# Performance work log

Measured on AMD Instinct MI355X. Metric: run time of the kernel, lower is better.

Reference implementation:

```python
import math
import jax, jax.numpy as jnp
import numpy as np

EPS = 1e-5
TEMP = 1.0
ROPE_BASE = 10000.0


def _ln(x, g, b):
    m = x.mean(-1, keepdims=True)
    v = ((x - m) ** 2).mean(-1, keepdims=True)
    return (x - m) / jnp.sqrt(v + EPS) * g + b


def _trigrams(n_heads):
    # 8 trigrams = all sign patterns of {-1,+1}^3, L2-normalized rows
    bits = ((np.arange(8)[:, None] >> np.arange(3)[None, :]) & 1).astype(np.float32)
    t = bits * 2.0 - 1.0
    t = t / np.linalg.norm(t, axis=1, keepdims=True)
    return jnp.asarray(t[:n_heads])  # [H, 3]


def _rope_tables(T, D):
    inv = 1.0 / (ROPE_BASE ** (np.arange(0, D, 2, dtype=np.float32) / D))
    ang = np.arange(T, dtype=np.float32)[:, None] * inv[None, :]  # [T, D/2]
    cos = np.concatenate([np.cos(ang), np.cos(ang)], axis=1)  # [T, D]
    sin = np.concatenate([np.sin(ang), np.sin(ang)], axis=1)
    return jnp.asarray(cos), jnp.asarray(sin)


def _apply_rope(x, cos, sin):
    # x: [B, H, T, D], rotate-half convention
    d = x.shape[-1] // 2
    rot = jnp.concatenate([-x[..., d:], x[..., :d]], axis=-1)
    return x * cos + rot * sin


def setup_inputs() -> dict:
    key = jax.random.key(0)
    ks = jax.random.split(key, 8)
    B, T, C, H = 2, 2048, 1024, 8
    FFN, QD = 4096, 6
    w = 0.02
    return {
        "x": jax.random.normal(ks[0], (B, T, C), jnp.float32),
        "ln_attn_g": jnp.ones((C,), jnp.float32),
        "ln_attn_b": jnp.zeros((C,), jnp.float32),
        "qkv_w": jax.random.normal(ks[1], (3 * C, C), jnp.float32) * w,
        "out_w": jax.random.normal(ks[2], (C, C), jnp.float32) * w,
        "head_scales": jax.random.normal(ks[3], (H,), jnp.float32) * 0.1,
        "ln_hex_g": jnp.ones((C,), jnp.float32),
        "ln_hex_b": jnp.zeros((C,), jnp.float32),
        "to_qd_w": jax.random.normal(ks[4], (QD, C), jnp.float32) * w,
        "from_qd_w": jax.random.normal(ks[5], (C, QD), jnp.float32) * w,
        "hex_scale": jnp.ones((1,), jnp.float32),
        "ln_ffn_g": jnp.ones((C,), jnp.float32),
        "ln_ffn_b": jnp.zeros((C,), jnp.float32),
        "ffn_w1": jax.random.normal(ks[6], (FFN, C), jnp.float32) * w,
        "ffn_b1": jnp.zeros((FFN,), jnp.float32),
        "ffn_w2": jax.random.normal(ks[7], (C, FFN), jnp.float32) * w,
        "ffn_b2": jnp.zeros((C,), jnp.float32),
    }


def _layer(x, ln_attn_g, ln_attn_b, qkv_w, out_w, head_scales,
           ln_hex_g, ln_hex_b, to_qd_w, from_qd_w, hex_scale,
           ln_ffn_g, ln_ffn_b, ffn_w1, ffn_b1, ffn_w2, ffn_b2):
    B, T, C = x.shape
    H = head_scales.shape[0]
    D = C // H

    # ---- attention with trigram geo-bias ----
    h = _ln(x, ln_attn_g, ln_attn_b)
    qkv = (h @ qkv_w.T).reshape(B, T, 3, H, D).transpose(2, 0, 3, 1, 4)
    q, k, v = qkv[0], qkv[1], qkv[2]  # [B, H, T, D]
    cos, sin = _rope_tables(T, D)
    q = _apply_rope(q, cos, sin)
    k = _apply_rope(k, cos, sin)

    mask = jnp.tril(jnp.ones((T, T), bool))
    scale = jnp.float32(1.0 / math.sqrt(D))
    scores = jnp.einsum('bhtd,bhsd->bhts', q, k) * scale
    scores = jnp.where(mask, scores, -jnp.inf)
    attn = jax.nn.softmax(scores, axis=-1)
    out = attn @ v  # [B, H, T, D]

    # rank-1 geometric correction (flash path)
    dirs = _trigrams(H)  # [H, 3]
    qp = jnp.einsum('bhtd,hd->bht', q[..., :3], dirs)
    kp = jnp.einsum('bhtd,hd->bht', k[..., :3], dirs)
    geo = qp[..., :, None] * kp[..., None, :]  # [B, H, T, T]
    geo_attn = jax.nn.softmax(jnp.where(mask, geo, -jnp.inf), axis=-1)
    geo_out = geo_attn @ v
    out = out + head_scales[None, :, None, None] * jax.lax.stop_gradient(geo_out - out)

    out = out.transpose(0, 2, 1, 3).reshape(B, T, C) @ out_w.T
    x = x + out

    # ---- hexagram VQ (factored6: per-dim binary quantize w/ straight-through) ----
    h = _ln(x, ln_hex_g, ln_hex_b)
    zq = h @ to_qd_w.T  # [B, T, 6]
    soft = jnp.tanh(zq / TEMP)
    hard = jnp.where(zq >= 0, 1.0, -1.0).astype(zq.dtype)
    zq_out = soft + jax.lax.stop_gradient(hard - soft)
    x = x + hex_scale[0] * (zq_out @ from_qd_w.T)

    # ---- FFN (GELU) ----
    h = _ln(x, ln_ffn_g, ln_ffn_b)
    x = x + (jax.nn.gelu(h @ ffn_w1.T + ffn_b1, approximate=False) @ ffn_w2.T + ffn_b2)
    return x


def reference(x, ln_attn_g, ln_attn_b, qkv_w, out_w, head_scales,
              ln_hex_g, ln_hex_b, to_qd_w, from_qd_w, hex_scale,
              ln_ffn_g, ln_ffn_b, ffn_w1, ffn_b1, ffn_w2, ffn_b2):
    return _layer(x, ln_attn_g, ln_attn_b, qkv_w, out_w, head_scales,
                  ln_hex_g, ln_hex_b, to_qd_w, from_qd_w, hex_scale,
                  ln_ffn_g, ln_ffn_b, ffn_w1, ffn_b1, ffn_w2, ffn_b2)
```

## Files before the change

### kernel.cpp

```cpp
#include <hip/hip_runtime.h>
#include <hip/hip_bf16.h>

typedef __attribute__((ext_vector_type(4))) float f32x4;
typedef __attribute__((ext_vector_type(8))) short short8;
typedef __attribute__((ext_vector_type(4))) short short4v;

namespace {

constexpr int Tt = 2048, Cc = 1024, Hh = 8, Dd = 128, FFNd = 4096;
constexpr int Bb = 2;
constexpr int Mrows = Bb * Tt;
constexpr float kNEG = -1e30f;
constexpr float L2E = 1.4426950408889634f;

static __device__ __forceinline__ float b2f(unsigned short u) {
  return __uint_as_float(((unsigned int)u) << 16);
}
static __device__ __forceinline__ unsigned short f2b(float f) {
  __hip_bfloat16 h = __float2bfloat16(f);
  unsigned short u;
  __builtin_memcpy(&u, &h, 2);
  return u;
}
static __device__ __forceinline__ void split2(float v, unsigned short& h, unsigned short& l) {
  h = f2b(v);
  float r = v - b2f(h);
  l = f2b(r);
}
static __device__ __forceinline__ void split3(float v, unsigned short& h, unsigned short& m,
                                              unsigned short& l) {
  h = f2b(v);
  float r = v - b2f(h);
  m = f2b(r);
  float r2 = r - b2f(m);
  l = f2b(r2);
}
static __device__ __forceinline__ float wave_sum(float v) {
#pragma unroll
  for (int m = 1; m < 64; m <<= 1) v += __shfl_xor(v, m);
  return v;
}
static __device__ __forceinline__ float grp16_sum(float v) {
#pragma unroll
  for (int m = 1; m < 16; m <<= 1) v += __shfl_xor(v, m);
  return v;
}
static __device__ __forceinline__ float grp16_max(float v) {
#pragma unroll
  for (int m = 1; m < 16; m <<= 1) v = fmaxf(v, __shfl_xor(v, m));
  return v;
}

__global__ __launch_bounds__(256) void cast_kernel(const float* __restrict__ in,
                                                   unsigned short* __restrict__ out, int n) {
  int i = (blockIdx.x * 256 + threadIdx.x) * 4;
  if (i + 3 < n) {
    float4 v = *(const float4*)&in[i];
    short4v o;
    o.x = (short)f2b(v.x);
    o.y = (short)f2b(v.y);
    o.z = (short)f2b(v.z);
    o.w = (short)f2b(v.w);
    *(short4v*)&out[i] = o;
  }
}

__global__ __launch_bounds__(256) void ln_kernel(const float* __restrict__ x,
                                                 const float* __restrict__ g,
                                                 const float* __restrict__ bb,
                                                 float* __restrict__ out) {
  int row = blockIdx.x * 4 + (threadIdx.x >> 6);
  int lane = threadIdx.x & 63;
  const float* xr = x + (size_t)row * Cc;
  float v[16];
  float s = 0.f;
#pragma unroll
  for (int c = 0; c < 4; ++c) {
    float4 t = *(const float4*)&xr[c * 256 + lane * 4];
    v[c * 4 + 0] = t.x; v[c * 4 + 1] = t.y; v[c * 4 + 2] = t.z; v[c * 4 + 3] = t.w;
    s += t.x + t.y + t.z + t.w;
  }
  s = wave_sum(s);
  float mean = s * (1.f / Cc);
  float s2 = 0.f;
#pragma unroll
  for (int j = 0; j < 16; ++j) {
    float d = v[j] - mean;
    s2 += d * d;
  }
  s2 = wave_sum(s2);
  float rstd = 1.0f / sqrtf(s2 * (1.f / Cc) + 1e-5f);
#pragma unroll
  for (int c = 0; c < 4; ++c) {
    float4 o;
#pragma unroll
    for (int j = 0; j < 4; ++j) {
      int idx = c * 256 + lane * 4 + j;
      ((float*)&o)[j] = (v[c * 4 + j] - mean) * rstd * g[idx] + bb[idx];
    }
    *(float4*)&out[(size_t)row * Cc + c * 256 + lane * 4] = o;
  }
}

template <int NS, int EPI>
__global__ __launch_bounds__(256) void gemm_sp(const float* __restrict__ A,
                                               const float* __restrict__ W,
                                               float* __restrict__ outF,
                                               unsigned short* __restrict__ outH,
                                               unsigned short* __restrict__ outL,
                                               const float* __restrict__ resid, int Nn, int Kk) {
  __shared__ __align__(16) unsigned short As[NS][128 * 32];
  __shared__ __align__(16) unsigned short Bs[NS][128 * 32];
  int m0 = blockIdx.x * 128, n0 = blockIdx.y * 128;
  int tid = threadIdx.x, lane = tid & 63, wid = tid >> 6;
  int wr = (wid >> 1) * 64, wc = (wid & 1) * 64;
  int g = lane >> 4, r16 = lane & 15;
  f32x4 acc[4][4];
#pragma unroll
  for (int mi = 0; mi < 4; ++mi)
#pragma unroll
    for (int ni = 0; ni < 4; ++ni) acc[mi][ni] = (f32x4){0.f, 0.f, 0.f, 0.f};
  for (int k0 = 0; k0 < Kk; k0 += 32) {
    __syncthreads();
#pragma unroll
    for (int it = 0; it < 4; ++it) {
      int chunk = tid + it * 256;
      int row = chunk >> 3, col4 = chunk & 7;
      int cc = col4 >> 1, half = col4 & 1;
      int off = row * 32 + ((cc ^ (row & 3)) * 8) + half * 4;
      float4 va = *(const float4*)&A[(size_t)(m0 + row) * Kk + k0 + col4 * 4];
      float4 vb = *(const float4*)&W[(size_t)(n0 + row) * Kk + k0 + col4 * 4];
      short4v sa[NS], sb[NS];
#pragma unroll
      for (int j = 0; j < 4; ++j) {
        unsigned short h, m, l;
        if constexpr (NS == 2) {
          split2(((float*)&va)[j], h, l);
          ((short*)&sa[0])[j] = (short)h; ((short*)&sa[1])[j] = (short)l;
          split2(((float*)&vb)[j], h, l);
          ((short*)&sb[0])[j] = (short)h; ((short*)&sb[1])[j] = (short)l;
        } else {
          split3(((float*)&va)[j], h, m, l);
          ((short*)&sa[0])[j] = (short)h; ((short*)&sa[1])[j] = (short)m; ((short*)&sa[2])[j] = (short)l;
          split3(((float*)&vb)[j], h, m, l);
          ((short*)&sb[0])[j] = (short)h; ((short*)&sb[1])[j] = (short)m; ((short*)&sb[2])[j] = (short)l;
        }
      }
#pragma unroll
      for (int s = 0; s < NS; ++s) {
        *(short4v*)&As[s][off] = sa[s];
        *(short4v*)&Bs[s][off] = sb[s];
      }
    }
    __syncthreads();
    short8 af[NS][4], bfv[NS][4];
#pragma unroll
    for (int mi = 0; mi < 4; ++mi) {
      int row = wr + mi * 16 + r16;
      int so = row * 32 + ((g ^ (row & 3)) * 8);
#pragma unroll
      for (int s = 0; s < NS; ++s) af[s][mi] = *(short8*)&As[s][so];
    }
#pragma unroll
    for (int ni = 0; ni < 4; ++ni) {
      int row = wc + ni * 16 + r16;
      int so = row * 32 + ((g ^ (row & 3)) * 8);
#pragma unroll
      for (int s = 0; s < NS; ++s) bfv[s][ni] = *(short8*)&Bs[s][so];
    }
    __builtin_amdgcn_s_setprio(1);
#pragma unroll
    for (int mi = 0; mi < 4; ++mi)
#pragma unroll
      for (int ni = 0; ni < 4; ++ni) {
        f32x4 a = acc[mi][ni];
        if constexpr (NS == 3) {
          a = __builtin_amdgcn_mfma_f32_16x16x32_bf16(af[1][mi], bfv[1][ni], a, 0, 0, 0);
          a = __builtin_amdgcn_mfma_f32_16x16x32_bf16(af[0][mi], bfv[2][ni], a, 0, 0, 0);
          a = __builtin_amdgcn_mfma_f32_16x16x32_bf16(af[2][mi], bfv[0][ni], a, 0, 0, 0);
        }
        a = __builtin_amdgcn_mfma_f32_16x16x32_bf16(af[0][mi], bfv[1][ni], a, 0, 0, 0);
        a = __builtin_amdgcn_mfma_f32_16x16x32_bf16(af[1][mi], bfv[0][ni], a, 0, 0, 0);
        a = __builtin_amdgcn_mfma_f32_16x16x32_bf16(af[0][mi], bfv[0][ni], a, 0, 0, 0);
        acc[mi][ni] = a;
      }
    __builtin_amdgcn_s_setprio(0);
  }
#pragma unroll
  for (int mi = 0; mi < 4; ++mi)
#pragma unroll
    for (int ni = 0; ni < 4; ++ni)
#pragma unroll
      for (int r = 0; r < 4; ++r) {
        int row = m0 + wr + mi * 16 + 4 * g + r;
        int col = n0 + wc + ni * 16 + r16;
        size_t o = (size_t)row * Nn + col;
        float v = acc[mi][ni][r];
        if constexpr (EPI == 0) {
          outF[o] = v;
        } else if constexpr (EPI == 1) {
          outF[o] = v + resid[o];
        } else {
          unsigned short hh, ll;
          split2(v, hh, ll);
          outH[o] = hh;
          outL[o] = ll;
        }
      }
}

template <int EPI>
__global__ __launch_bounds__(256) void gemm_bt(const unsigned short* __restrict__ A,
                                               const unsigned short* __restrict__ W,
                                               float* __restrict__ outF,
                                               unsigned short* __restrict__ outB,
                                               const float* __restrict__ bias,
                                               const float* __restrict__ resid, int Nn, int Kk) {
  __shared__ __align__(16) unsigned short As[128 * 32];
  __shared__ __align__(16) unsigned short Bs[128 * 32];
  int m0 = blockIdx.x * 128, n0 = blockIdx.y * 128;
  int tid = threadIdx.x, lane = tid & 63, wid = tid >> 6;
  int wr = (wid >> 1) * 64, wc = (wid & 1) * 64;
  int g = lane >> 4, r16 = lane & 15;
  f32x4 acc[4][4];
#pragma unroll
  for (int mi = 0; mi < 4; ++mi)
#pragma unroll
    for (int ni = 0; ni < 4; ++ni) acc[mi][ni] = (f32x4){0.f, 0.f, 0.f, 0.f};
  for (int k0 = 0; k0 < Kk; k0 += 32) {
    __syncthreads();
#pragma unroll
    for (int c = 0; c < 2; ++c) {
      int chunk = tid + c * 256;
      int row = chunk >> 2, cc = chunk & 3;
      int sw = cc ^ (row & 3);
      *(short8*)&As[row * 32 + sw * 8] = *(const short8*)&A[(size_t)(m0 + row) * Kk + k0 + cc * 8];
      *(short8*)&Bs[row * 32 + sw * 8] = *(const short8*)&W[(size_t)(n0 + row) * Kk + k0 + cc * 8];
    }
    __syncthreads();
    short8 af[4], bfr[4];
#pragma unroll
    for (int mi = 0; mi < 4; ++mi) {
      int row = wr + mi * 16 + r16;
      af[mi] = *(short8*)&As[row * 32 + ((g ^ (row & 3)) * 8)];
    }
#pragma unroll
    for (int ni = 0; ni < 4; ++ni) {
      int row = wc + ni * 16 + r16;
      bfr[ni] = *(short8*)&Bs[row * 32 + ((g ^ (row & 3)) * 8)];
    }
    __builtin_amdgcn_s_setprio(1);
#pragma unroll
    for (int mi = 0; mi < 4; ++mi)
#pragma unroll
      for (int ni = 0; ni < 4; ++ni)
        acc[mi][ni] = __builtin_amdgcn_mfma_f32_16x16x32_bf16(af[mi], bfr[ni], acc[mi][ni], 0, 0, 0);
    __builtin_amdgcn_s_setprio(0);
  }
#pragma unroll
  for (int mi = 0; mi < 4; ++mi)
#pragma unroll
    for (int ni = 0; ni < 4; ++ni)
#pragma unroll
      for (int r = 0; r < 4; ++r) {
        int row = m0 + wr + mi * 16 + 4 * g + r;
        int col = n0 + wc + ni * 16 + r16;
        size_t o = (size_t)row * Nn + col;
        float v = acc[mi][ni][r];
        if constexpr (EPI == 2) {
          v += bias[col];
          v = 0.5f * v * (1.f + erff(v * 0.70710678118654752f));
          outB[o] = f2b(v);
        } else {
          v += bias[col];
          outF[o] = v + resid[o];
        }
      }
}

__global__ __launch_bounds__(256) void rope_table(float* __restrict__ ct, float* __restrict__ st) {
  int idx = blockIdx.x * 256 + threadIdx.x;
  int t = idx >> 6, i = idx & 63;
  float e = (float)i * (1.f / 64.f);
  float p = powf(10000.0f, e);
  float inv = 1.0f / p;
  float ang = (float)t * inv;
  ct[idx] = cosf(ang);
  st[idx] = sinf(ang);
}

__global__ __launch_bounds__(256) void rope_apply(unsigned short* __restrict__ qkvh,
                                                  unsigned short* __restrict__ qkvl,
                                                  unsigned short* __restrict__ khsw,
                                                  unsigned short* __restrict__ klsw,
                                                  const float* __restrict__ ct,
                                                  const float* __restrict__ st,
                                                  float* __restrict__ qp, float* __restrict__ kp) {
  int w = blockIdx.x * 4 + (threadIdx.x >> 6);
  int lane = threadIdx.x & 63;
  int b = w / (Hh * Tt);
  int rem = w % (Hh * Tt);
  int h = rem / Tt;
  int t = rem % Tt;
  size_t base = ((size_t)(b * Tt + t)) * 3 * Cc + h * Dd;
  float cv = ct[t * 64 + lane], sv = st[t * 64 + lane];
  float q_lo = b2f(qkvh[base + lane]) + b2f(qkvl[base + lane]);
  float q_hi = b2f(qkvh[base + lane + 64]) + b2f(qkvl[base + lane + 64]);
  float qn_lo = q_lo * cv - q_hi * sv;
  float qn_hi = q_hi * cv + q_lo * sv;
  unsigned short hh, ll;
  split2(qn_lo, hh, ll);
  qkvh[base + lane] = hh; qkvl[base + lane] = ll;
  split2(qn_hi, hh, ll);
  qkvh[base + lane + 64] = hh; qkvl[base + lane + 64] = ll;
  size_t kbase = base + Cc;
  float k_lo = b2f(qkvh[kbase + lane]) + b2f(qkvl[kbase + lane]);
  float k_hi = b2f(qkvh[kbase + lane + 64]) + b2f(qkvl[kbase + lane + 64]);
  float kn_lo = k_lo * cv - k_hi * sv;
  float kn_hi = k_hi * cv + k_lo * sv;
  size_t krow = ((size_t)(b * Hh + h) * Tt + t) * 128;
  int tsw = t & 7;
  int d0 = lane, d1 = lane + 64;
  int c0 = (((d0 >> 3) ^ tsw) << 3) | (d0 & 7);
  int c1 = (((d1 >> 3) ^ tsw) << 3) | (d1 & 7);
  split2(kn_lo, hh, ll);
  khsw[krow + c0] = hh; klsw[krow + c0] = ll;
  split2(kn_hi, hh, ll);
  khsw[krow + c1] = hh; klsw[krow + c1] = ll;
  float t0 = (((h >> 0) & 1) ? 1.f : -1.f) * 0.57735026918962576f;
  float t1 = (((h >> 1) & 1) ? 1.f : -1.f) * 0.57735026918962576f;
  float t2 = (((h >> 2) & 1) ? 1.f : -1.f) * 0.57735026918962576f;
  float q0v = __shfl(qn_lo, 0), q1v = __shfl(qn_lo, 1), q2v = __shfl(qn_lo, 2);
  float k0v = __shfl(kn_lo, 0), k1v = __shfl(kn_lo, 1), k2v = __shfl(kn_lo, 2);
  if (lane == 0) {
    qp[(size_t)(b * Hh + h) * Tt + t] = q0v * t0 + q1v * t1 + q2v * t2;
    kp[(size_t)(b * Hh + h) * Tt + t] = k0v * t0 + k1v * t1 + k2v * t2;
  }
}

__global__ __launch_bounds__(256) void vtrans(const unsigned short* __restrict__ qkvh,
                                              const unsigned short* __restrict__ qkvl,
                                              unsigned short* __restrict__ vth,
                                              unsigned short* __restrict__ vtl) {
  __shared__ unsigned short Lh[64 * 68], Ll[64 * 68];
  int bidx = blockIdx.x;
  int dd = bidx & 1;
  int tt = (bidx >> 1) & 31;
  int bh = bidx >> 6;
  int b = bh >> 3, h = bh & 7;
  int tid = threadIdx.x;
#pragma unroll
  for (int it = 0; it < 2; ++it) {
    int chunk = tid + it * 256;
    int tr = chunk >> 3, c8 = chunk & 7;
    size_t src = ((size_t)(b * Tt + tt * 64 + tr)) * 3 * Cc + 2 * Cc + h * Dd + dd * 64 + c8 * 8;
    short8 vh = *(const short8*)&qkvh[src];
    short8 vl = *(const short8*)&qkvl[src];
    *(short4v*)&Lh[tr * 68 + c8 * 8] = *(short4v*)&vh;
    *(short4v*)&Lh[tr * 68 + c8 * 8 + 4] = *((short4v*)&vh + 1);
    *(short4v*)&Ll[tr * 68 + c8 * 8] = *(short4v*)&vl;
    *(short4v*)&Ll[tr * 68 + c8 * 8 + 4] = *((short4v*)&vl + 1);
  }
  __syncthreads();
#pragma unroll
  for (int it = 0; it < 2; ++it) {
    int chunk = tid + it * 256;
    int dr = chunk >> 3, t8 = chunk & 7;
    short8 oh, ol;
#pragma unroll
    for (int e = 0; e < 8; ++e) {
      oh[e] = (short)Lh[(t8 * 8 + e) * 68 + dr];
      ol[e] = (short)Ll[(t8 * 8 + e) * 68 + dr];
    }
    size_t dst = ((size_t)(bh * Dd + dd * 64 + dr)) * Tt + tt * 64 + t8 * 8;
    *(short8*)&vth[dst] = oh;
    *(short8*)&vtl[dst] = ol;
  }
}

__global__ __launch_bounds__(256) void attn_fused(const unsigned short* __restrict__ qkvh,
                                                  const unsigned short* __restrict__ qkvl,
                                                  const unsigned short* __restrict__ khsw,
                                                  const unsigned short* __restrict__ klsw,
                                                  const unsigned short* __restrict__ vth,
                                                  const unsigned short* __restrict__ vtl,
                                                  const float* __restrict__ qp,
                                                  const float* __restrict__ kp,
                                                  const float* __restrict__ head_scales,
                                                  float* __restrict__ out) {
  int i = blockIdx.x;
  int bh = i & 15;
  int j = i >> 4;
  int qblk = (j < 16) ? (31 - j) : (j - 16);
  int b = bh >> 3, h = bh & 7;
  int q0 = qblk * 64;
  int tid = threadIdx.x, lane = tid & 63, wid = tid >> 6;
  int wq0 = q0 + wid * 16;
  int g = lane >> 4, r16 = lane & 15;
  __shared__ __align__(16) unsigned short Ksh[32 * 128], Ksl[32 * 128];
  __shared__ __align__(16) unsigned short Vsh[128 * 40], Vsl[128 * 40];
  __shared__ __align__(16) unsigned short PsAh[4][512], PsAl[4][512];
  __shared__ __align__(16) unsigned short PsGh[4][512], PsGl[4][512];

  short8 qh[4], ql[4];
#pragma unroll
  for (int c = 0; c < 4; ++c) {
    size_t qoff = (size_t)(b * Tt + wq0 + r16) * 3 * Cc + h * Dd + c * 32 + g * 8;
    qh[c] = *(const short8*)&qkvh[qoff];
    ql[c] = *(const short8*)&qkvl[qoff];
  }

  float hs = head_scales[h];
  const float* qpb = qp + (size_t)bh * Tt;
  const float* kpb = kp + (size_t)bh * Tt;
  float qpv[4];
#pragma unroll
  for (int r = 0; r < 4; ++r) qpv[r] = qpb[wq0 + 4 * g + r] * L2E;

  f32x4 accA[8], accG[8];
#pragma unroll
  for (int n = 0; n < 8; ++n) {
    accA[n] = (f32x4){0.f, 0.f, 0.f, 0.f};
    accG[n] = (f32x4){0.f, 0.f, 0.f, 0.f};
  }
  float m1[4], l1[4], m2[4], l2[4];
#pragma unroll
  for (int r = 0; r < 4; ++r) { m1[r] = kNEG; l1[r] = 0.f; m2[r] = kNEG; l2[r] = 0.f; }

  const float scale2 = 0.08838834764831845f * L2E;

  const unsigned short* Khb = khsw + (size_t)bh * Tt * 128;
  const unsigned short* Klb = klsw + (size_t)bh * Tt * 128;
  const unsigned short* Vhb = vth + (size_t)bh * Dd * Tt;
  const unsigned short* Vlb = vtl + (size_t)bh * Dd * Tt;

  for (int s0 = 0; s0 < q0 + 64; s0 += 32) {
    __syncthreads();
#pragma unroll
    for (int it = 0; it < 2; ++it) {
      int chunk = tid + it * 256;
      int row = chunk >> 4, c8 = chunk & 15;
      size_t src = (size_t)(s0 + row) * 128 + c8 * 8;
      *(short8*)&Ksh[row * 128 + c8 * 8] = *(const short8*)&Khb[src];
      *(short8*)&Ksl[row * 128 + c8 * 8] = *(const short8*)&Klb[src];
    }
#pragma unroll
    for (int it = 0; it < 2; ++it) {
      int chunk = tid + it * 256;
      int d = chunk >> 2, k8 = chunk & 3;
      size_t src = (size_t)d * Tt + s0 + k8 * 8;
      *(short8*)&Vsh[d * 40 + k8 * 8] = *(const short8*)&Vhb[src];
      *(short8*)&Vsl[d * 40 + k8 * 8] = *(const short8*)&Vlb[src];
    }
    __syncthreads();
    if (s0 <= wq0 + 15) {
      f32x4 sf[2];
      sf[0] = (f32x4){0.f, 0.f, 0.f, 0.f};
      sf[1] = (f32x4){0.f, 0.f, 0.f, 0.f};
      __builtin_amdgcn_s_setprio(1);
#pragma unroll
      for (int st2 = 0; st2 < 2; ++st2) {
        int row = st2 * 16 + r16;
        int rsw = row & 7;
#pragma unroll
        for (int c = 0; c < 4; ++c) {
          int off = row * 128 + (((c * 4 + g) ^ rsw) * 8);
          short8 kh = *(short8*)&Ksh[off];
          short8 kl = *(short8*)&Ksl[off];
          sf[st2] = __builtin_amdgcn_mfma_f32_16x16x32_bf16(ql[c], kh, sf[st2], 0, 0, 0);
          sf[st2] = __builtin_amdgcn_mfma_f32_16x16x32_bf16(qh[c], kl, sf[st2], 0, 0, 0);
          sf[st2] = __builtin_amdgcn_mfma_f32_16x16x32_bf16(qh[c], kh, sf[st2], 0, 0, 0);
        }
      }
      __builtin_amdgcn_s_setprio(0);
      float kpv2[2];
      kpv2[0] = kpb[s0 + r16];
      kpv2[1] = kpb[s0 + 16 + r16];
      float pA[2][4], pG[2][4], scl1[4], scl2[4];
#pragma unroll
      for (int r = 0; r < 4; ++r) {
        int qi = wq0 + 4 * g + r;
        bool ok0 = (s0 + r16) <= qi;
        bool ok1 = (s0 + 16 + r16) <= qi;
        float sv0 = ok0 ? sf[0][r] * scale2 : kNEG;
        float sv1 = ok1 ? sf[1][r] * scale2 : kNEG;
        float tm = grp16_max(fmaxf(sv0, sv1));
        float mn = fmaxf(m1[r], tm);
        float sc = exp2f(m1[r] - mn);
        float p0 = ok0 ? exp2f(sv0 - mn) : 0.f;
        float p1 = ok1 ? exp2f(sv1 - mn) : 0.f;
        l1[r] = l1[r] * sc + grp16_sum(p0 + p1);
        m1[r] = mn; scl1[r] = sc; pA[0][r] = p0; pA[1][r] = p1;
        float gv0 = qpv[r] * kpv2[0];
        float gv1 = qpv[r] * kpv2[1];
        float g0 = ok0 ? gv0 : kNEG;
        float g1 = ok1 ? gv1 : kNEG;
        float tg = grp16_max(fmaxf(g0, g1));
        float mg = fmaxf(m2[r], tg);
        float sg = exp2f(m2[r] - mg);
        float pg0 = ok0 ? exp2f(g0 - mg) : 0.f;
        float pg1 = ok1 ? exp2f(g1 - mg) : 0.f;
        l2[r] = l2[r] * sg + grp16_sum(pg0 + pg1);
        m2[r] = mg; scl2[r] = sg; pG[0][r] = pg0; pG[1][r] = pg1;
      }
#pragma unroll
      for (int n = 0; n < 8; ++n)
#pragma unroll
        for (int r = 0; r < 4; ++r) {
          accA[n][r] *= scl1[r];
          accG[n][r] *= scl2[r];
        }
#pragma unroll
      for (int st2 = 0; st2 < 2; ++st2)
#pragma unroll
        for (int r = 0; r < 4; ++r) {
          int rowp = 4 * g + r;
          int cbase = st2 * 2 + (r16 >> 3);
          int cs = cbase ^ (rowp & 3);
          int off = rowp * 32 + cs * 8 + (r16 & 7);
          unsigned short hh, ll;
          split2(pA[st2][r], hh, ll);
          PsAh[wid][off] = hh; PsAl[wid][off] = ll;
          split2(pG[st2][r], hh, ll);
          PsGh[wid][off] = hh; PsGl[wid][off] = ll;
        }
      int po = r16 * 32 + ((g ^ (r16 & 3)) * 8);
      short8 aph = *(short8*)&PsAh[wid][po];
      short8 apl = *(short8*)&PsAl[wid][po];
      short8 agh = *(short8*)&PsGh[wid][po];
      short8 agl = *(short8*)&PsGl[wid][po];
      __builtin_amdgcn_s_setprio(1);
#pragma unroll
      for (int n = 0; n < 8; ++n) {
        int vo = (n * 16 + r16) * 40 + g * 8;
        short8 bvh = *(short8*)&Vsh[vo];
        short8 bvl = *(short8*)&Vsl[vo];
        accA[n] = __builtin_amdgcn_mfma_f32_16x16x32_bf16(apl, bvh, accA[n], 0, 0, 0);
        accA[n] = __builtin_amdgcn_mfma_f32_16x16x32_bf16(aph, bvl, accA[n], 0, 0, 0);
        accA[n] = __builtin_amdgcn_mfma_f32_16x16x32_bf16(aph, bvh, accA[n], 0, 0, 0);
        accG[n] = __builtin_amdgcn_mfma_f32_16x16x32_bf16(agl, bvh, accG[n], 0, 0, 0);
        accG[n] = __builtin_amdgcn_mfma_f32_16x16x32_bf16(agh, bvl, accG[n], 0, 0, 0);
        accG[n] = __builtin_amdgcn_mfma_f32_16x16x32_bf16(agh, bvh, accG[n], 0, 0, 0);
      }
      __builtin_amdgcn_s_setprio(0);
    }
  }
#pragma unroll
  for (int n = 0; n < 8; ++n)
#pragma unroll
    for (int r = 0; r < 4; ++r) {
      int qi = wq0 + 4 * g + r;
      float av = accA[n][r] / l1[r];
      float gv = accG[n][r] / l2[r];
      out[(size_t)(b * Tt + qi) * Cc + h * Dd + n * 16 + r16] = av + hs * (gv - av);
    }
}

__global__ __launch_bounds__(256) void hex_kernel(float* __restrict__ x1,
                                                  const float* __restrict__ hg,
                                                  const float* __restrict__ hb,
                                                  const float* __restrict__ to_qd,
                                                  const float* __restrict__ from_qd,
                                                  const float* __restrict__ hex_scale,
                                                  const float* __restrict__ fg,
                                                  const float* __restrict__ fb,
                                                  unsigned short* __restrict__ h_ffn) {
  int row = blockIdx.x * 4 + (threadIdx.x >> 6);
  int lane = threadIdx.x & 63;
  float* xr = x1 + (size_t)row * Cc;
  float v[16];
  float s = 0.f;
#pragma unroll
  for (int c = 0; c < 4; ++c) {
    float4 t = *(const float4*)&xr[c * 256 + lane * 4];
    v[c * 4 + 0] = t.x; v[c * 4 + 1] = t.y; v[c * 4 + 2] = t.z; v[c * 4 + 3] = t.w;
    s += t.x + t.y + t.z + t.w;
  }
  s = wave_sum(s);
  float mean = s * (1.f / Cc);
  float s2 = 0.f;
#pragma unroll
  for (int j = 0; j < 16; ++j) { float d = v[j] - mean; s2 += d * d; }
  s2 = wave_sum(s2);
  float rstd = 1.0f / sqrtf(s2 * (1.f / Cc) + 1e-5f);
  float zq[6] = {0.f, 0.f, 0.f, 0.f, 0.f, 0.f};
#pragma unroll
  for (int c = 0; c < 4; ++c)
#pragma unroll
    for (int j2 = 0; j2 < 4; ++j2) {
      int idx = c * 256 + lane * 4 + j2;
      float hv = (v[c * 4 + j2] - mean) * rstd * hg[idx] + hb[idx];
#pragma unroll
      for (int j = 0; j < 6; ++j) zq[j] += hv * to_qd[j * Cc + idx];
    }
#pragma unroll
  for (int j = 0; j < 6; ++j) zq[j] = wave_sum(zq[j]);
  float hsc = hex_scale[0];
  float hard[6];
#pragma unroll
  for (int j = 0; j < 6; ++j) hard[j] = (zq[j] >= 0.f) ? hsc : -hsc;
  float x2v[16];
  float t1 = 0.f;
#pragma unroll
  for (int c = 0; c < 4; ++c)
#pragma unroll
    for (int j2 = 0; j2 < 4; ++j2) {
      int idx = c * 256 + lane * 4 + j2;
      float a = 0.f;
#pragma unroll
      for (int j = 0; j < 6; ++j) a += hard[j] * from_qd[idx * 6 + j];
      float xv = v[c * 4 + j2] + a;
      x2v[c * 4 + j2] = xv;
      t1 += xv;
    }
  t1 = wave_sum(t1);
  float mean2 = t1 * (1.f / Cc);
  float t2 = 0.f;
#pragma unroll
  for (int j = 0; j < 16; ++j) { float d = x2v[j] - mean2; t2 += d * d; }
  t2 = wave_sum(t2);
  float rstd2 = 1.0f / sqrtf(t2 * (1.f / Cc) + 1e-5f);
#pragma unroll
  for (int c = 0; c < 4; ++c) {
    float4 t;
    t.x = x2v[c * 4 + 0]; t.y = x2v[c * 4 + 1]; t.z = x2v[c * 4 + 2]; t.w = x2v[c * 4 + 3];
    *(float4*)&xr[c * 256 + lane * 4] = t;
    short4v o;
#pragma unroll
    for (int j = 0; j < 4; ++j) {
      int idx = c * 256 + lane * 4 + j;
      ((short*)&o)[j] = (short)f2b((x2v[c * 4 + j] - mean2) * rstd2 * fg[idx] + fb[idx]);
    }
    *(short4v*)&h_ffn[(size_t)row * Cc + c * 256 + lane * 4] = o;
  }
}

}

extern "C" void kernel_launch(void* const* d_in, const int* in_sizes, int n_in, void* d_out,
                              int out_size, void* d_ws, size_t ws_size, hipStream_t stream) {
  const float* x = (const float*)d_in[0];
  const float* ln_attn_g = (const float*)d_in[1];
  const float* ln_attn_b = (const float*)d_in[2];
  const float* qkv_w = (const float*)d_in[3];
  const float* out_w = (const float*)d_in[4];
  const float* head_scales = (const float*)d_in[5];
  const float* ln_hex_g = (const float*)d_in[6];
  const float* ln_hex_b = (const float*)d_in[7];
  const float* to_qd_w = (const float*)d_in[8];
  const float* from_qd_w = (const float*)d_in[9];
  const float* hex_scale = (const float*)d_in[10];
  const float* ln_ffn_g = (const float*)d_in[11];
  const float* ln_ffn_b = (const float*)d_in[12];
  const float* ffn_w1 = (const float*)d_in[13];
  const float* ffn_b1 = (const float*)d_in[14];
  const float* ffn_w2 = (const float*)d_in[15];
  const float* ffn_b2 = (const float*)d_in[16];

  char* ws = (char*)d_ws;
  size_t off = 0;
  auto alloc = [&](size_t bytes) -> char* {
    char* p = ws + off;
    off += (bytes + 255) & ~(size_t)255;
    return p;
  };
  char* regA = alloc((size_t)Mrows * 3 * Cc * 2 * 2);
  unsigned short* qkvh = (unsigned short*)regA;
  unsigned short* qkvl = qkvh + (size_t)Mrows * 3 * Cc;
  unsigned short* gelu = (unsigned short*)regA;
  float* x1 = (float*)(regA + (size_t)Mrows * FFNd * 2);
  char* regB = alloc((size_t)Mrows * Cc * 4);
  float* h = (float*)regB;
  unsigned short* khsw = (unsigned short*)regB;
  unsigned short* klsw = khsw + (size_t)Bb * Hh * Tt * 128;
  char* regC = alloc((size_t)Bb * Hh * Dd * Tt * 2 * 2);
  unsigned short* vth = (unsigned short*)regC;
  unsigned short* vtl = vth + (size_t)Bb * Hh * Dd * Tt;
  unsigned short* w1_b = (unsigned short*)regC;
  unsigned short* w2_b = w1_b + (size_t)FFNd * Cc;
  char* regD = alloc((size_t)Mrows * Cc * 4);
  float* attn_out = (float*)regD;
  unsigned short* h_ffn = (unsigned short*)regD;
  float* ct = (float*)alloc((size_t)Tt * 64 * 4);
  float* st = (float*)alloc((size_t)Tt * 64 * 4);
  float* qp = (float*)alloc((size_t)Bb * Hh * Tt * 4);
  float* kp = (float*)alloc((size_t)Bb * Hh * Tt * 4);

  ln_kernel<<<Mrows / 4, 256, 0, stream>>>(x, ln_attn_g, ln_attn_b, h);
  gemm_sp<2, 2><<<dim3(Mrows / 128, (3 * Cc) / 128), 256, 0, stream>>>(h, qkv_w, nullptr, qkvh,
                                                                       qkvl, nullptr, 3 * Cc, Cc);
  rope_table<<<(Tt * 64) / 256, 256, 0, stream>>>(ct, st);
  rope_apply<<<(Bb * Hh * Tt) / 4, 256, 0, stream>>>(qkvh, qkvl, khsw, klsw, ct, st, qp, kp);
  vtrans<<<Bb * Hh * 32 * 2, 256, 0, stream>>>(qkvh, qkvl, vth, vtl);
  attn_fused<<<Bb * Hh * (Tt / 64), 256, 0, stream>>>(qkvh, qkvl, khsw, klsw, vth, vtl, qp, kp,
                                                      head_scales, attn_out);
  gemm_sp<3, 1><<<dim3(Mrows / 128, Cc / 128), 256, 0, stream>>>(attn_out, out_w, x1, nullptr,
                                                                 nullptr, x, Cc, Cc);
  hex_kernel<<<Mrows / 4, 256, 0, stream>>>(x1, ln_hex_g, ln_hex_b, to_qd_w, from_qd_w, hex_scale,
                                            ln_ffn_g, ln_ffn_b, h_ffn);
  cast_kernel<<<(FFNd * Cc) / 1024, 256, 0, stream>>>(ffn_w1, w1_b, FFNd * Cc);
  cast_kernel<<<(Cc * FFNd) / 1024, 256, 0, stream>>>(ffn_w2, w2_b, Cc * FFNd);
  gemm_bt<2><<<dim3(Mrows / 128, FFNd / 128), 256, 0, stream>>>(h_ffn, w1_b, nullptr, gelu,
                                                                ffn_b1, nullptr, FFNd, Cc);
  gemm_bt<3><<<dim3(Mrows / 128, Cc / 128), 256, 0, stream>>>(gelu, w2_b, (float*)d_out, nullptr,
                                                              ffn_b2, x1, Cc, FFNd);
}
```

Before: 663.0 us.

## Pre-split operands into bf16 planes and rewrite attention with register prefetch

The split-precision GEMMs now take pre-split bf16 hi/lo(/mid) planes instead of splitting fp32 tiles inside the k-loop. LayerNorm, the weights and the attention output are split by separate kernels, and the QKV epilogue writes separate Q/K/V planes. Attention is rewritten: it prefetches K/V tiles into registers, uses a different softmax bookkeeping, sets launch bounds to 2 blocks per CU and writes a 3-way split output. This removes repeated per-tile conversion work and cuts LDS traffic, but adds extra kernel launches and more global memory traffic for the split planes.

```diff
diff --git a/kernel.cpp b/kernel.cpp
--- a/kernel.cpp
+++ b/kernel.cpp
@@ -40,16 +40,6 @@
   for (int m = 1; m < 64; m <<= 1) v += __shfl_xor(v, m);
   return v;
 }
-static __device__ __forceinline__ float grp16_sum(float v) {
-#pragma unroll
-  for (int m = 1; m < 16; m <<= 1) v += __shfl_xor(v, m);
-  return v;
-}
-static __device__ __forceinline__ float grp16_max(float v) {
-#pragma unroll
-  for (int m = 1; m < 16; m <<= 1) v = fmaxf(v, __shfl_xor(v, m));
-  return v;
-}
 
 __global__ __launch_bounds__(256) void cast_kernel(const float* __restrict__ in,
                                                    unsigned short* __restrict__ out, int n) {
@@ -57,18 +47,52 @@
   if (i + 3 < n) {
     float4 v = *(const float4*)&in[i];
     short4v o;
-    o.x = (short)f2b(v.x);
-    o.y = (short)f2b(v.y);
-    o.z = (short)f2b(v.z);
-    o.w = (short)f2b(v.w);
+    o.x = (short)f2b(v.x); o.y = (short)f2b(v.y); o.z = (short)f2b(v.z); o.w = (short)f2b(v.w);
     *(short4v*)&out[i] = o;
   }
 }
-
-__global__ __launch_bounds__(256) void ln_kernel(const float* __restrict__ x,
-                                                 const float* __restrict__ g,
-                                                 const float* __restrict__ bb,
-                                                 float* __restrict__ out) {
+__global__ __launch_bounds__(256) void wsplit2_k(const float* __restrict__ in,
+                                                 unsigned short* __restrict__ o0,
+                                                 unsigned short* __restrict__ o1, int n) {
+  int i = (blockIdx.x * 256 + threadIdx.x) * 4;
+  if (i + 3 < n) {
+    float4 v = *(const float4*)&in[i];
+    short4v a, b;
+#pragma unroll
+    for (int j = 0; j < 4; ++j) {
+      unsigned short hh, ll;
+      split2(((float*)&v)[j], hh, ll);
+      a[j] = (short)hh; b[j] = (short)ll;
+    }
+    *(short4v*)&o0[i] = a;
+    *(short4v*)&o1[i] = b;
+  }
+}
+__global__ __launch_bounds__(256) void wsplit3_k(const float* __restrict__ in,
+                                                 unsigned short* __restrict__ o0,
+                                                 unsigned short* __restrict__ o1,
+                                                 unsigned short* __restrict__ o2, int n) {
+  int i = (blockIdx.x * 256 + threadIdx.x) * 4;
+  if (i + 3 < n) {
+    float4 v = *(const float4*)&in[i];
+    short4v a, b, c;
+#pragma unroll
+    for (int j = 0; j < 4; ++j) {
+      unsigned short hh, mm, ll;
+      split3(((float*)&v)[j], hh, mm, ll);
+      a[j] = (short)hh; b[j] = (short)mm; c[j] = (short)ll;
+    }
+    *(short4v*)&o0[i] = a;
+    *(short4v*)&o1[i] = b;
+    *(short4v*)&o2[i] = c;
+  }
+}
+
+__global__ __launch_bounds__(256) void ln_split(const float* __restrict__ x,
+                                                const float* __restrict__ g,
+                                                const float* __restrict__ bb,
+                                                unsigned short* __restrict__ oh,
+                                                unsigned short* __restrict__ ol) {
   int row = blockIdx.x * 4 + (threadIdx.x >> 6);
   int lane = threadIdx.x & 63;
   const float* xr = x + (size_t)row * Cc;
@@ -84,37 +108,40 @@
   float mean = s * (1.f / Cc);
   float s2 = 0.f;
 #pragma unroll
-  for (int j = 0; j < 16; ++j) {
-    float d = v[j] - mean;
-    s2 += d * d;
-  }
+  for (int j = 0; j < 16; ++j) { float d = v[j] - mean; s2 += d * d; }
   s2 = wave_sum(s2);
   float rstd = 1.0f / sqrtf(s2 * (1.f / Cc) + 1e-5f);
 #pragma unroll
   for (int c = 0; c < 4; ++c) {
-    float4 o;
+    short4v a, b;
 #pragma unroll
     for (int j = 0; j < 4; ++j) {
       int idx = c * 256 + lane * 4 + j;
-      ((float*)&o)[j] = (v[c * 4 + j] - mean) * rstd * g[idx] + bb[idx];
-    }
-    *(float4*)&out[(size_t)row * Cc + c * 256 + lane * 4] = o;
+      float hv = (v[c * 4 + j] - mean) * rstd * g[idx] + bb[idx];
+      unsigned short hh, ll;
+      split2(hv, hh, ll);
+      a[j] = (short)hh; b[j] = (short)ll;
+    }
+    *(short4v*)&oh[(size_t)row * Cc + c * 256 + lane * 4] = a;
+    *(short4v*)&ol[(size_t)row * Cc + c * 256 + lane * 4] = b;
   }
 }
 
 template <int NS, int EPI>
-__global__ __launch_bounds__(256) void gemm_sp(const float* __restrict__ A,
-                                               const float* __restrict__ W,
-                                               float* __restrict__ outF,
-                                               unsigned short* __restrict__ outH,
-                                               unsigned short* __restrict__ outL,
-                                               const float* __restrict__ resid, int Nn, int Kk) {
+__global__ __launch_bounds__(256) void gemm_pn(
+    const unsigned short* __restrict__ A0, const unsigned short* __restrict__ A1,
+    const unsigned short* __restrict__ A2, const unsigned short* __restrict__ W0,
+    const unsigned short* __restrict__ W1, const unsigned short* __restrict__ W2,
+    unsigned short* __restrict__ outP, size_t planeStride, float* __restrict__ outF,
+    const float* __restrict__ resid, int Nn, int Kk) {
   __shared__ __align__(16) unsigned short As[NS][128 * 32];
   __shared__ __align__(16) unsigned short Bs[NS][128 * 32];
   int m0 = blockIdx.x * 128, n0 = blockIdx.y * 128;
   int tid = threadIdx.x, lane = tid & 63, wid = tid >> 6;
   int wr = (wid >> 1) * 64, wc = (wid & 1) * 64;
   int g = lane >> 4, r16 = lane & 15;
+  const unsigned short* Aps[3] = {A0, A1, A2};
+  const unsigned short* Wps[3] = {W0, W1, W2};
   f32x4 acc[4][4];
 #pragma unroll
   for (int mi = 0; mi < 4; ++mi)
@@ -123,35 +150,15 @@
   for (int k0 = 0; k0 < Kk; k0 += 32) {
     __syncthreads();
 #pragma unroll
-    for (int it = 0; it < 4; ++it) {
-      int chunk = tid + it * 256;
-      int row = chunk >> 3, col4 = chunk & 7;
-      int cc = col4 >> 1, half = col4 & 1;
-      int off = row * 32 + ((cc ^ (row & 3)) * 8) + half * 4;
-      float4 va = *(const float4*)&A[(size_t)(m0 + row) * Kk + k0 + col4 * 4];
-      float4 vb = *(const float4*)&W[(size_t)(n0 + row) * Kk + k0 + col4 * 4];
-      short4v sa[NS], sb[NS];
-#pragma unroll
-      for (int j = 0; j < 4; ++j) {
-        unsigned short h, m, l;
-        if constexpr (NS == 2) {
-          split2(((float*)&va)[j], h, l);
-          ((short*)&sa[0])[j] = (short)h; ((short*)&sa[1])[j] = (short)l;
-          split2(((float*)&vb)[j], h, l);
-          ((short*)&sb[0])[j] = (short)h; ((short*)&sb[1])[j] = (short)l;
-        } else {
-          split3(((float*)&va)[j], h, m, l);
-          ((short*)&sa[0])[j] = (short)h; ((short*)&sa[1])[j] = (short)m; ((short*)&sa[2])[j] = (short)l;
-          split3(((float*)&vb)[j], h, m, l);
-          ((short*)&sb[0])[j] = (short)h; ((short*)&sb[1])[j] = (short)m; ((short*)&sb[2])[j] = (short)l;
-        }
+    for (int s = 0; s < NS; ++s)
+#pragma unroll
+      for (int it = 0; it < 2; ++it) {
+        int slot = it * 256 + tid;
+        int row = slot >> 2, sw = slot & 3;
+        int cc = sw ^ (row & 3);
+        *(short8*)&As[s][slot * 8] = *(const short8*)&Aps[s][(size_t)(m0 + row) * Kk + k0 + cc * 8];
+        *(short8*)&Bs[s][slot * 8] = *(const short8*)&Wps[s][(size_t)(n0 + row) * Kk + k0 + cc * 8];
       }
-#pragma unroll
-      for (int s = 0; s < NS; ++s) {
-        *(short4v*)&As[s][off] = sa[s];
-        *(short4v*)&Bs[s][off] = sb[s];
-      }
-    }
     __syncthreads();
     short8 af[NS][4], bfv[NS][4];
 #pragma unroll
@@ -194,17 +201,16 @@
       for (int r = 0; r < 4; ++r) {
         int row = m0 + wr + mi * 16 + 4 * g + r;
         int col = n0 + wc + ni * 16 + r16;
-        size_t o = (size_t)row * Nn + col;
         float v = acc[mi][ni][r];
         if constexpr (EPI == 0) {
-          outF[o] = v;
-        } else if constexpr (EPI == 1) {
-          outF[o] = v + resid[o];
-        } else {
+          int sec = col >> 10, cw = col & 1023;
           unsigned short hh, ll;
           split2(v, hh, ll);
-          outH[o] = hh;
-          outL[o] = ll;
+          outP[(size_t)(2 * sec) * planeStride + (size_t)row * Cc + cw] = hh;
+          outP[(size_t)(2 * sec + 1) * planeStride + (size_t)row * Cc + cw] = ll;
+        } else {
+          size_t o = (size_t)row * Nn + col;
+          outF[o] = v + resid[o];
         }
       }
 }
@@ -289,8 +295,10 @@
   st[idx] = sinf(ang);
 }
 
-__global__ __launch_bounds__(256) void rope_apply(unsigned short* __restrict__ qkvh,
-                                                  unsigned short* __restrict__ qkvl,
+__global__ __launch_bounds__(256) void rope_apply(unsigned short* __restrict__ qh_p,
+                                                  unsigned short* __restrict__ ql_p,
+                                                  const unsigned short* __restrict__ kh_p,
+                                                  const unsigned short* __restrict__ kl_p,
                                                   unsigned short* __restrict__ khsw,
                                                   unsigned short* __restrict__ klsw,
                                                   const float* __restrict__ ct,
@@ -302,20 +310,19 @@
   int rem = w % (Hh * Tt);
   int h = rem / Tt;
   int t = rem % Tt;
-  size_t base = ((size_t)(b * Tt + t)) * 3 * Cc + h * Dd;
+  size_t base = (size_t)(b * Tt + t) * Cc + h * Dd;
   float cv = ct[t * 64 + lane], sv = st[t * 64 + lane];
-  float q_lo = b2f(qkvh[base + lane]) + b2f(qkvl[base + lane]);
-  float q_hi = b2f(qkvh[base + lane + 64]) + b2f(qkvl[base + lane + 64]);
+  float q_lo = b2f(qh_p[base + lane]) + b2f(ql_p[base + lane]);
+  float q_hi = b2f(qh_p[base + lane + 64]) + b2f(ql_p[base + lane + 64]);
   float qn_lo = q_lo * cv - q_hi * sv;
   float qn_hi = q_hi * cv + q_lo * sv;
   unsigned short hh, ll;
   split2(qn_lo, hh, ll);
-  qkvh[base + lane] = hh; qkvl[base + lane] = ll;
+  qh_p[base + lane] = hh; ql_p[base + lane] = ll;
   split2(qn_hi, hh, ll);
-  qkvh[base + lane + 64] = hh; qkvl[base + lane + 64] = ll;
-  size_t kbase = base + Cc;
-  float k_lo = b2f(qkvh[kbase + lane]) + b2f(qkvl[kbase + lane]);
-  float k_hi = b2f(qkvh[kbase + lane + 64]) + b2f(qkvl[kbase + lane + 64]);
+  qh_p[base + lane + 64] = hh; ql_p[base + lane + 64] = ll;
+  float k_lo = b2f(kh_p[base + lane]) + b2f(kl_p[base + lane]);
+  float k_hi = b2f(kh_p[base + lane + 64]) + b2f(kl_p[base + lane + 64]);
   float kn_lo = k_lo * cv - k_hi * sv;
   float kn_hi = k_hi * cv + k_lo * sv;
   size_t krow = ((size_t)(b * Hh + h) * Tt + t) * 128;
@@ -338,8 +345,8 @@
   }
 }
 
-__global__ __launch_bounds__(256) void vtrans(const unsigned short* __restrict__ qkvh,
-                                              const unsigned short* __restrict__ qkvl,
+__global__ __launch_bounds__(256) void vtrans(const unsigned short* __restrict__ vh_p,
+                                              const unsigned short* __restrict__ vl_p,
                                               unsigned short* __restrict__ vth,
                                               unsigned short* __restrict__ vtl) {
   __shared__ unsigned short Lh[64 * 68], Ll[64 * 68];
@@ -353,9 +360,9 @@
   for (int it = 0; it < 2; ++it) {
     int chunk = tid + it * 256;
     int tr = chunk >> 3, c8 = chunk & 7;
-    size_t src = ((size_t)(b * Tt + tt * 64 + tr)) * 3 * Cc + 2 * Cc + h * Dd + dd * 64 + c8 * 8;
-    short8 vh = *(const short8*)&qkvh[src];
-    short8 vl = *(const short8*)&qkvl[src];
+    size_t src = (size_t)(b * Tt + tt * 64 + tr) * Cc + h * Dd + dd * 64 + c8 * 8;
+    short8 vh = *(const short8*)&vh_p[src];
+    short8 vl = *(const short8*)&vl_p[src];
     *(short4v*)&Lh[tr * 68 + c8 * 8] = *(short4v*)&vh;
     *(short4v*)&Lh[tr * 68 + c8 * 8 + 4] = *((short4v*)&vh + 1);
     *(short4v*)&Ll[tr * 68 + c8 * 8] = *(short4v*)&vl;
@@ -372,187 +379,208 @@
       oh[e] = (short)Lh[(t8 * 8 + e) * 68 + dr];
       ol[e] = (short)Ll[(t8 * 8 + e) * 68 + dr];
     }
-    size_t dst = ((size_t)(bh * Dd + dd * 64 + dr)) * Tt + tt * 64 + t8 * 8;
+    size_t dst = (size_t)(bh * Dd + dd * 64 + dr) * Tt + tt * 64 + t8 * 8;
     *(short8*)&vth[dst] = oh;
     *(short8*)&vtl[dst] = ol;
   }
 }
 
-__global__ __launch_bounds__(256) void attn_fused(const unsigned short* __restrict__ qkvh,
-                                                  const unsigned short* __restrict__ qkvl,
-                                                  const unsigned short* __restrict__ khsw,
-                                                  const unsigned short* __restrict__ klsw,
-                                                  const unsigned short* __restrict__ vth,
-                                                  const unsigned short* __restrict__ vtl,
-                                                  const float* __restrict__ qp,
-                                                  const float* __restrict__ kp,
-                                                  const float* __restrict__ head_scales,
-                                                  float* __restrict__ out) {
-  int i = blockIdx.x;
-  int bh = i & 15;
-  int j = i >> 4;
-  int qblk = (j < 16) ? (31 - j) : (j - 16);
+__global__ __launch_bounds__(256, 2) void attn_v3(
+    const unsigned short* __restrict__ qh_p, const unsigned short* __restrict__ ql_p,
+    const unsigned short* __restrict__ khsw, const unsigned short* __restrict__ klsw,
+    const unsigned short* __restrict__ vth, const unsigned short* __restrict__ vtl,
+    const float* __restrict__ qp, const float* __restrict__ kp,
+    const float* __restrict__ head_scales, unsigned short* __restrict__ ao0,
+    unsigned short* __restrict__ ao1, unsigned short* __restrict__ ao2) {
+  int cix = blockIdx.x & 255, rix = blockIdx.x >> 8;
+  int bh = cix >> 4, ii = cix & 15;
+  int qblk = rix ? ii : 31 - ii;
   int b = bh >> 3, h = bh & 7;
   int q0 = qblk * 64;
   int tid = threadIdx.x, lane = tid & 63, wid = tid >> 6;
   int wq0 = q0 + wid * 16;
   int g = lane >> 4, r16 = lane & 15;
   __shared__ __align__(16) unsigned short Ksh[32 * 128], Ksl[32 * 128];
-  __shared__ __align__(16) unsigned short Vsh[128 * 40], Vsl[128 * 40];
-  __shared__ __align__(16) unsigned short PsAh[4][512], PsAl[4][512];
-  __shared__ __align__(16) unsigned short PsGh[4][512], PsGl[4][512];
-
-  short8 qh[4], ql[4];
-#pragma unroll
-  for (int c = 0; c < 4; ++c) {
-    size_t qoff = (size_t)(b * Tt + wq0 + r16) * 3 * Cc + h * Dd + c * 32 + g * 8;
-    qh[c] = *(const short8*)&qkvh[qoff];
-    ql[c] = *(const short8*)&qkvl[qoff];
-  }
-
+  __shared__ __align__(16) unsigned short Vsh[128 * 34], Vsl[128 * 34];
+
+  short8 qfh[4], qfl[4];
+#pragma unroll
+  for (int c4 = 0; c4 < 4; ++c4) {
+    size_t qoff = (size_t)(b * Tt + wq0 + r16) * Cc + h * Dd + c4 * 32 + g * 8;
+    qfh[c4] = *(const short8*)&qh_p[qoff];
+    qfl[c4] = *(const short8*)&ql_p[qoff];
+  }
   float hs = head_scales[h];
-  const float* qpb = qp + (size_t)bh * Tt;
   const float* kpb = kp + (size_t)bh * Tt;
-  float qpv[4];
-#pragma unroll
-  for (int r = 0; r < 4; ++r) qpv[r] = qpb[wq0 + 4 * g + r] * L2E;
-
-  f32x4 accA[8], accG[8];
-#pragma unroll
-  for (int n = 0; n < 8; ++n) {
-    accA[n] = (f32x4){0.f, 0.f, 0.f, 0.f};
-    accG[n] = (f32x4){0.f, 0.f, 0.f, 0.f};
-  }
-  float m1[4], l1[4], m2[4], l2[4];
-#pragma unroll
-  for (int r = 0; r < 4; ++r) { m1[r] = kNEG; l1[r] = 0.f; m2[r] = kNEG; l2[r] = 0.f; }
-
-  const float scale2 = 0.08838834764831845f * L2E;
+  float qpl2 = qp[(size_t)bh * Tt + wq0 + r16] * L2E;
 
   const unsigned short* Khb = khsw + (size_t)bh * Tt * 128;
   const unsigned short* Klb = klsw + (size_t)bh * Tt * 128;
   const unsigned short* Vhb = vth + (size_t)bh * Dd * Tt;
   const unsigned short* Vlb = vtl + (size_t)bh * Dd * Tt;
 
-  for (int s0 = 0; s0 < q0 + 64; s0 += 32) {
+  f32x4 accA[8], accG[8];
+#pragma unroll
+  for (int n = 0; n < 8; ++n) {
+    accA[n] = (f32x4){0.f, 0.f, 0.f, 0.f};
+    accG[n] = (f32x4){0.f, 0.f, 0.f, 0.f};
+  }
+  float m1 = kNEG, l1 = 0.f, m2 = kNEG, l2 = 0.f;
+  const float scale2 = 0.08838834764831845f * L2E;
+
+  int nt = 2 * qblk + 2;
+  short8 rkh[2], rkl[2], rvh[2], rvl[2];
+  int krw[2], kcl[2], vdd[2], vkk[2];
+#pragma unroll
+  for (int it = 0; it < 2; ++it) {
+    int chunk = tid + it * 256;
+    krw[it] = chunk >> 4; kcl[it] = (chunk & 15) * 8;
+    vdd[it] = chunk >> 2; vkk[it] = (chunk & 3) * 8;
+  }
+  auto LOADT = [&](int s0) {
+#pragma unroll
+    for (int it = 0; it < 2; ++it) {
+      size_t ksrc = (size_t)(s0 + krw[it]) * 128 + kcl[it];
+      rkh[it] = *(const short8*)&Khb[ksrc];
+      rkl[it] = *(const short8*)&Klb[ksrc];
+      size_t vsrc = (size_t)vdd[it] * Tt + s0 + vkk[it];
+      rvh[it] = *(const short8*)&Vhb[vsrc];
+      rvl[it] = *(const short8*)&Vlb[vsrc];
+    }
+  };
+  LOADT(0);
+  for (int t = 0; t < nt; ++t) {
+    int s0 = t * 32;
     __syncthreads();
 #pragma unroll
     for (int it = 0; it < 2; ++it) {
-      int chunk = tid + it * 256;
-      int row = chunk >> 4, c8 = chunk & 15;
-      size_t src = (size_t)(s0 + row) * 128 + c8 * 8;
-      *(short8*)&Ksh[row * 128 + c8 * 8] = *(const short8*)&Khb[src];
-      *(short8*)&Ksl[row * 128 + c8 * 8] = *(const short8*)&Klb[src];
-    }
-#pragma unroll
-    for (int it = 0; it < 2; ++it) {
-      int chunk = tid + it * 256;
-      int d = chunk >> 2, k8 = chunk & 3;
-      size_t src = (size_t)d * Tt + s0 + k8 * 8;
-      *(short8*)&Vsh[d * 40 + k8 * 8] = *(const short8*)&Vhb[src];
-      *(short8*)&Vsl[d * 40 + k8 * 8] = *(const short8*)&Vlb[src];
+      *(short8*)&Ksh[krw[it] * 128 + kcl[it]] = rkh[it];
+      *(short8*)&Ksl[krw[it] * 128 + kcl[it]] = rkl[it];
+      *(short8*)&Vsh[vdd[it] * 34 + vkk[it]] = rvh[it];
+      *(short8*)&Vsl[vdd[it] * 34 + vkk[it]] = rvl[it];
     }
     __syncthreads();
-    if (s0 <= wq0 + 15) {
-      f32x4 sf[2];
-      sf[0] = (f32x4){0.f, 0.f, 0.f, 0.f};
-      sf[1] = (f32x4){0.f, 0.f, 0.f, 0.f};
-      __builtin_amdgcn_s_setprio(1);
-#pragma unroll
-      for (int st2 = 0; st2 < 2; ++st2) {
-        int row = st2 * 16 + r16;
-        int rsw = row & 7;
-#pragma unroll
-        for (int c = 0; c < 4; ++c) {
-          int off = row * 128 + (((c * 4 + g) ^ rsw) * 8);
-          short8 kh = *(short8*)&Ksh[off];
-          short8 kl = *(short8*)&Ksl[off];
-          sf[st2] = __builtin_amdgcn_mfma_f32_16x16x32_bf16(ql[c], kh, sf[st2], 0, 0, 0);
-          sf[st2] = __builtin_amdgcn_mfma_f32_16x16x32_bf16(qh[c], kl, sf[st2], 0, 0, 0);
-          sf[st2] = __builtin_amdgcn_mfma_f32_16x16x32_bf16(qh[c], kh, sf[st2], 0, 0, 0);
-        }
+    if (t + 1 < nt) LOADT(s0 + 32);
+    if (s0 > wq0 + 15) continue;
+    float kpv[2][4];
+#pragma unroll
+    for (int st2 = 0; st2 < 2; ++st2)
+#pragma unroll
+      for (int rr = 0; rr < 4; ++rr) kpv[st2][rr] = kpb[s0 + st2 * 16 + 4 * g + rr];
+    f32x4 sf[2];
+    sf[0] = (f32x4){0.f, 0.f, 0.f, 0.f};
+    sf[1] = (f32x4){0.f, 0.f, 0.f, 0.f};
+    __builtin_amdgcn_s_setprio(1);
+#pragma unroll
+    for (int st2 = 0; st2 < 2; ++st2) {
+      int row = st2 * 16 + r16, rsw = row & 7;
+#pragma unroll
+      for (int c4 = 0; c4 < 4; ++c4) {
+        int off = row * 128 + (((c4 * 4 + g) ^ rsw) * 8);
+        short8 kh8 = *(short8*)&Ksh[off];
+        short8 kl8 = *(short8*)&Ksl[off];
+        sf[st2] = __builtin_amdgcn_mfma_f32_16x16x32_bf16(kl8, qfh[c4], sf[st2], 0, 0, 0);
+        sf[st2] = __builtin_amdgcn_mfma_f32_16x16x32_bf16(kh8, qfl[c4], sf[st2], 0, 0, 0);
+        sf[st2] = __builtin_amdgcn_mfma_f32_16x16x32_bf16(kh8, qfh[c4], sf[st2], 0, 0, 0);
       }
-      __builtin_amdgcn_s_setprio(0);
-      float kpv2[2];
-      kpv2[0] = kpb[s0 + r16];
-      kpv2[1] = kpb[s0 + 16 + r16];
-      float pA[2][4], pG[2][4], scl1[4], scl2[4];
-#pragma unroll
-      for (int r = 0; r < 4; ++r) {
-        int qi = wq0 + 4 * g + r;
-        bool ok0 = (s0 + r16) <= qi;
-        bool ok1 = (s0 + 16 + r16) <= qi;
-        float sv0 = ok0 ? sf[0][r] * scale2 : kNEG;
-        float sv1 = ok1 ? sf[1][r] * scale2 : kNEG;
-        float tm = grp16_max(fmaxf(sv0, sv1));
-        float mn = fmaxf(m1[r], tm);
-        float sc = exp2f(m1[r] - mn);
-        float p0 = ok0 ? exp2f(sv0 - mn) : 0.f;
-        float p1 = ok1 ? exp2f(sv1 - mn) : 0.f;
-        l1[r] = l1[r] * sc + grp16_sum(p0 + p1);
-        m1[r] = mn; scl1[r] = sc; pA[0][r] = p0; pA[1][r] = p1;
-        float gv0 = qpv[r] * kpv2[0];
-        float gv1 = qpv[r] * kpv2[1];
-        float g0 = ok0 ? gv0 : kNEG;
-        float g1 = ok1 ? gv1 : kNEG;
-        float tg = grp16_max(fmaxf(g0, g1));
-        float mg = fmaxf(m2[r], tg);
-        float sg = exp2f(m2[r] - mg);
-        float pg0 = ok0 ? exp2f(g0 - mg) : 0.f;
-        float pg1 = ok1 ? exp2f(g1 - mg) : 0.f;
-        l2[r] = l2[r] * sg + grp16_sum(pg0 + pg1);
-        m2[r] = mg; scl2[r] = sg; pG[0][r] = pg0; pG[1][r] = pg1;
+    }
+    __builtin_amdgcn_s_setprio(0);
+    bool okf[2][4];
+    float sv[2][4], gvv[2][4];
+    float mx = kNEG, gmx = kNEG;
+#pragma unroll
+    for (int st2 = 0; st2 < 2; ++st2)
+#pragma unroll
+      for (int rr = 0; rr < 4; ++rr) {
+        int key = s0 + st2 * 16 + 4 * g + rr;
+        bool ok = key <= wq0 + r16;
+        okf[st2][rr] = ok;
+        float s = ok ? sf[st2][rr] * scale2 : kNEG;
+        sv[st2][rr] = s;
+        mx = fmaxf(mx, s);
+        float gg = ok ? qpl2 * kpv[st2][rr] : kNEG;
+        gvv[st2][rr] = gg;
+        gmx = fmaxf(gmx, gg);
       }
-#pragma unroll
-      for (int n = 0; n < 8; ++n)
-#pragma unroll
-        for (int r = 0; r < 4; ++r) {
-          accA[n][r] *= scl1[r];
-          accG[n][r] *= scl2[r];
-        }
-#pragma unroll
-      for (int st2 = 0; st2 < 2; ++st2)
-#pragma unroll
-        for (int r = 0; r < 4; ++r) {
-          int rowp = 4 * g + r;
-          int cbase = st2 * 2 + (r16 >> 3);
-          int cs = cbase ^ (rowp & 3);
-          int off = rowp * 32 + cs * 8 + (r16 & 7);
-          unsigned short hh, ll;
-          split2(pA[st2][r], hh, ll);
-          PsAh[wid][off] = hh; PsAl[wid][off] = ll;
-          split2(pG[st2][r], hh, ll);
-          PsGh[wid][off] = hh; PsGl[wid][off] = ll;
-        }
-      int po = r16 * 32 + ((g ^ (r16 & 3)) * 8);
-      short8 aph = *(short8*)&PsAh[wid][po];
-      short8 apl = *(short8*)&PsAl[wid][po];
-      short8 agh = *(short8*)&PsGh[wid][po];
-      short8 agl = *(short8*)&PsGl[wid][po];
-      __builtin_amdgcn_s_setprio(1);
-#pragma unroll
-      for (int n = 0; n < 8; ++n) {
-        int vo = (n * 16 + r16) * 40 + g * 8;
-        short8 bvh = *(short8*)&Vsh[vo];
-        short8 bvl = *(short8*)&Vsl[vo];
-        accA[n] = __builtin_amdgcn_mfma_f32_16x16x32_bf16(apl, bvh, accA[n], 0, 0, 0);
-        accA[n] = __builtin_amdgcn_mfma_f32_16x16x32_bf16(aph, bvl, accA[n], 0, 0, 0);
-        accA[n] = __builtin_amdgcn_mfma_f32_16x16x32_bf16(aph, bvh, accA[n], 0, 0, 0);
-        accG[n] = __builtin_amdgcn_mfma_f32_16x16x32_bf16(agl, bvh, accG[n], 0, 0, 0);
-        accG[n] = __builtin_amdgcn_mfma_f32_16x16x32_bf16(agh, bvl, accG[n], 0, 0, 0);
-        accG[n] = __builtin_amdgcn_mfma_f32_16x16x32_bf16(agh, bvh, accG[n], 0, 0, 0);
+    mx = fmaxf(mx, __shfl_xor(mx, 16));
+    mx = fmaxf(mx, __shfl_xor(mx, 32));
+    gmx = fmaxf(gmx, __shfl_xor(gmx, 16));
+    gmx = fmaxf(gmx, __shfl_xor(gmx, 32));
+    float mn = fmaxf(m1, mx), sc = exp2f(m1 - mn);
+    float mg = fmaxf(m2, gmx), sg = exp2f(m2 - mg);
+    float pa[2][4], pgv[2][4];
+    float ps = 0.f, pgs = 0.f;
+#pragma unroll
+    for (int st2 = 0; st2 < 2; ++st2)
+#pragma unroll
+      for (int rr = 0; rr < 4; ++rr) {
+        float p = okf[st2][rr] ? exp2f(sv[st2][rr] - mn) : 0.f;
+        pa[st2][rr] = p; ps += p;
+        float pq = okf[st2][rr] ? exp2f(gvv[st2][rr] - mg) : 0.f;
+        pgv[st2][rr] = pq; pgs += pq;
       }
-      __builtin_amdgcn_s_setprio(0);
-    }
+    ps += __shfl_xor(ps, 16); ps += __shfl_xor(ps, 32);
+    pgs += __shfl_xor(pgs, 16); pgs += __shfl_xor(pgs, 32);
+    l1 = l1 * sc + ps; m1 = mn;
+    l2 = l2 * sg + pgs; m2 = mg;
+    float sclA[4], sclG[4];
+#pragma unroll
+    for (int rr = 0; rr < 4; ++rr) {
+      sclA[rr] = __shfl(sc, 4 * g + rr);
+      sclG[rr] = __shfl(sg, 4 * g + rr);
+    }
+#pragma unroll
+    for (int n = 0; n < 8; ++n)
+#pragma unroll
+      for (int rr = 0; rr < 4; ++rr) {
+        accA[n][rr] *= sclA[rr];
+        accG[n][rr] *= sclG[rr];
+      }
+    short8 pAh, pAl, pGh, pGl;
+#pragma unroll
+    for (int e = 0; e < 8; ++e) {
+      unsigned short hh, ll;
+      split2(pa[e >> 2][e & 3], hh, ll);
+      pAh[e] = (short)hh; pAl[e] = (short)ll;
+      split2(pgv[e >> 2][e & 3], hh, ll);
+      pGh[e] = (short)hh; pGl[e] = (short)ll;
+    }
+    __builtin_amdgcn_s_setprio(1);
+#pragma unroll
+    for (int n = 0; n < 8; ++n) {
+      int dofs = (n * 16 + r16) * 34;
+      short8 vh8, vl8;
+      *(short4v*)&vh8 = *(short4v*)&Vsh[dofs + 4 * g];
+      *((short4v*)&vh8 + 1) = *(short4v*)&Vsh[dofs + 16 + 4 * g];
+      *(short4v*)&vl8 = *(short4v*)&Vsl[dofs + 4 * g];
+      *((short4v*)&vl8 + 1) = *(short4v*)&Vsl[dofs + 16 + 4 * g];
+      accA[n] = __builtin_amdgcn_mfma_f32_16x16x32_bf16(pAl, vh8, accA[n], 0, 0, 0);
+      accA[n] = __builtin_amdgcn_mfma_f32_16x16x32_bf16(pAh, vl8, accA[n], 0, 0, 0);
+      accA[n] = __builtin_amdgcn_mfma_f32_16x16x32_bf16(pAh, vh8, accA[n], 0, 0, 0);
+      accG[n] = __builtin_amdgcn_mfma_f32_16x16x32_bf16(pGl, vh8, accG[n], 0, 0, 0);
+      accG[n] = __builtin_amdgcn_mfma_f32_16x16x32_bf16(pGh, vl8, accG[n], 0, 0, 0);
+      accG[n] = __builtin_amdgcn_mfma_f32_16x16x32_bf16(pGh, vh8, accG[n], 0, 0, 0);
+    }
+    __builtin_amdgcn_s_setprio(0);
+  }
+  float lA[4], lG[4];
+#pragma unroll
+  for (int rr = 0; rr < 4; ++rr) {
+    lA[rr] = __shfl(l1, 4 * g + rr);
+    lG[rr] = __shfl(l2, 4 * g + rr);
   }
 #pragma unroll
   for (int n = 0; n < 8; ++n)
 #pragma unroll
-    for (int r = 0; r < 4; ++r) {
-      int qi = wq0 + 4 * g + r;
-      float av = accA[n][r] / l1[r];
-      float gv = accG[n][r] / l2[r];
-      out[(size_t)(b * Tt + qi) * Cc + h * Dd + n * 16 + r16] = av + hs * (gv - av);
+    for (int rr = 0; rr < 4; ++rr) {
+      int qi = wq0 + 4 * g + rr;
+      float av = accA[n][rr] / lA[rr];
+      float gq = accG[n][rr] / lG[rr];
+      float o = av + hs * (gq - av);
+      unsigned short s1, s2v, s3;
+      split3(o, s1, s2v, s3);
+      size_t oo = (size_t)(b * Tt + qi) * Cc + h * Dd + n * 16 + r16;
+      ao0[oo] = s1; ao1[oo] = s2v; ao2[oo] = s3;
     }
 }
 
@@ -657,51 +685,58 @@
   const float* ffn_w2 = (const float*)d_in[15];
   const float* ffn_b2 = (const float*)d_in[16];
 
-  char* ws = (char*)d_ws;
-  size_t off = 0;
-  auto alloc = [&](size_t bytes) -> char* {
-    char* p = ws + off;
-    off += (bytes + 255) & ~(size_t)255;
-    return p;
-  };
-  char* regA = alloc((size_t)Mrows * 3 * Cc * 2 * 2);
-  unsigned short* qkvh = (unsigned short*)regA;
-  unsigned short* qkvl = qkvh + (size_t)Mrows * 3 * Cc;
-  unsigned short* gelu = (unsigned short*)regA;
-  float* x1 = (float*)(regA + (size_t)Mrows * FFNd * 2);
-  char* regB = alloc((size_t)Mrows * Cc * 4);
-  float* h = (float*)regB;
-  unsigned short* khsw = (unsigned short*)regB;
-  unsigned short* klsw = khsw + (size_t)Bb * Hh * Tt * 128;
-  char* regC = alloc((size_t)Bb * Hh * Dd * Tt * 2 * 2);
-  unsigned short* vth = (unsigned short*)regC;
-  unsigned short* vtl = vth + (size_t)Bb * Hh * Dd * Tt;
-  unsigned short* w1_b = (unsigned short*)regC;
-  unsigned short* w2_b = w1_b + (size_t)FFNd * Cc;
-  char* regD = alloc((size_t)Mrows * Cc * 4);
-  float* attn_out = (float*)regD;
-  unsigned short* h_ffn = (unsigned short*)regD;
-  float* ct = (float*)alloc((size_t)Tt * 64 * 4);
-  float* st = (float*)alloc((size_t)Tt * 64 * 4);
-  float* qp = (float*)alloc((size_t)Bb * Hh * Tt * 4);
-  float* kp = (float*)alloc((size_t)Bb * Hh * Tt * 4);
-
-  ln_kernel<<<Mrows / 4, 256, 0, stream>>>(x, ln_attn_g, ln_attn_b, h);
-  gemm_sp<2, 2><<<dim3(Mrows / 128, (3 * Cc) / 128), 256, 0, stream>>>(h, qkv_w, nullptr, qkvh,
-                                                                       qkvl, nullptr, 3 * Cc, Cc);
+  unsigned short* ws16 = (unsigned short*)d_ws;
+  const size_t PL = (size_t)Mrows * Cc;
+  unsigned short* hh = ws16 + 0 * PL;
+  unsigned short* hl = ws16 + 1 * PL;
+  unsigned short* qhp = ws16 + 2 * PL;
+  unsigned short* qlp = ws16 + 3 * PL;
+  unsigned short* khp = ws16 + 4 * PL;
+  unsigned short* klp = ws16 + 5 * PL;
+  unsigned short* vhp = ws16 + 6 * PL;
+  unsigned short* vlp = ws16 + 7 * PL;
+  unsigned short* khsw = ws16 + 8 * PL;
+  unsigned short* klsw = ws16 + 9 * PL;
+  unsigned short* vth = ws16 + 10 * PL;
+  unsigned short* vtl = ws16 + 11 * PL;
+  float* tail = (float*)(ws16 + 12 * PL);
+  float* ct = tail;
+  float* st = ct + (size_t)Tt * 64;
+  float* qp = st + (size_t)Tt * 64;
+  float* kp = qp + (size_t)Bb * Hh * Tt;
+  unsigned short* ao0 = hh;
+  unsigned short* ao1 = hl;
+  unsigned short* ao2 = khp;
+  float* x1 = (float*)klp;
+  unsigned short* h_ffn = vlp;
+  unsigned short* w1b = qhp;
+  unsigned short* w2b = qlp;
+  unsigned short* gelu = khsw;
+  unsigned short* wqh = vth;
+  unsigned short* wql = vtl;
+  unsigned short* ow0 = khsw;
+  unsigned short* ow1 = khsw + (size_t)Cc * Cc;
+  unsigned short* ow2 = khsw + (size_t)2 * Cc * Cc;
+
+  ln_split<<<Mrows / 4, 256, 0, stream>>>(x, ln_attn_g, ln_attn_b, hh, hl);
+  wsplit2_k<<<(3 * Cc * Cc) / 1024, 256, 0, stream>>>(qkv_w, wqh, wql, 3 * Cc * Cc);
+  gemm_pn<2, 0><<<dim3(Mrows / 128, (3 * Cc) / 128), 256, 0, stream>>>(
+      hh, hl, nullptr, wqh, wql, nullptr, qhp, PL, nullptr, nullptr, 3 * Cc, Cc);
   rope_table<<<(Tt * 64) / 256, 256, 0, stream>>>(ct, st);
-  rope_apply<<<(Bb * Hh * Tt) / 4, 256, 0, stream>>>(qkvh, qkvl, khsw, klsw, ct, st, qp, kp);
-  vtrans<<<Bb * Hh * 32 * 2, 256, 0, stream>>>(qkvh, qkvl, vth, vtl);
-  attn_fused<<<Bb * Hh * (Tt / 64), 256, 0, stream>>>(qkvh, qkvl, khsw, klsw, vth, vtl, qp, kp,
-                                                      head_scales, attn_out);
-  gemm_sp<3, 1><<<dim3(Mrows / 128, Cc / 128), 256, 0, stream>>>(attn_out, out_w, x1, nullptr,
-                                                                 nullptr, x, Cc, Cc);
+  rope_apply<<<(Bb * Hh * Tt) / 4, 256, 0, stream>>>(qhp, qlp, khp, klp, khsw, klsw, ct, st, qp,
+                                                     kp);
+  vtrans<<<Bb * Hh * 32 * 2, 256, 0, stream>>>(vhp, vlp, vth, vtl);
+  attn_v3<<<512, 256, 0, stream>>>(qhp, qlp, khsw, klsw, vth, vtl, qp, kp, head_scales, ao0, ao1,
+                                   ao2);
+  wsplit3_k<<<(Cc * Cc) / 1024, 256, 0, stream>>>(out_w, ow0, ow1, ow2, Cc * Cc);
+  gemm_pn<3, 1><<<dim3(Mrows / 128, Cc / 128), 256, 0, stream>>>(
+      ao0, ao1, ao2, ow0, ow1, ow2, nullptr, 0, x1, x, Cc, Cc);
   hex_kernel<<<Mrows / 4, 256, 0, stream>>>(x1, ln_hex_g, ln_hex_b, to_qd_w, from_qd_w, hex_scale,
                                             ln_ffn_g, ln_ffn_b, h_ffn);
-  cast_kernel<<<(FFNd * Cc) / 1024, 256, 0, stream>>>(ffn_w1, w1_b, FFNd * Cc);
-  cast_kernel<<<(Cc * FFNd) / 1024, 256, 0, stream>>>(ffn_w2, w2_b, Cc * FFNd);
-  gemm_bt<2><<<dim3(Mrows / 128, FFNd / 128), 256, 0, stream>>>(h_ffn, w1_b, nullptr, gelu,
-                                                                ffn_b1, nullptr, FFNd, Cc);
-  gemm_bt<3><<<dim3(Mrows / 128, Cc / 128), 256, 0, stream>>>(gelu, w2_b, (float*)d_out, nullptr,
+  cast_kernel<<<(FFNd * Cc) / 1024, 256, 0, stream>>>(ffn_w1, w1b, FFNd * Cc);
+  cast_kernel<<<(Cc * FFNd) / 1024, 256, 0, stream>>>(ffn_w2, w2b, Cc * FFNd);
+  gemm_bt<2><<<dim3(Mrows / 128, FFNd / 128), 256, 0, stream>>>(h_ffn, w1b, nullptr, gelu, ffn_b1,
+                                                                nullptr, FFNd, Cc);
+  gemm_bt<3><<<dim3(Mrows / 128, Cc / 128), 256, 0, stream>>>(gelu, w2b, (float*)d_out, nullptr,
                                                               ffn_b2, x1, Cc, FFNd);
 }
```

New measurement: 542.7 us. 18.1% less time.
